# Kernel tuning notes

Hardware: AMD Instinct MI355X
Metric: run time of the kernel (lower is better)

Reference implementation:

```python
import jax, jax.numpy as jnp
import numpy as np
import math

D_MODEL, D_STATE, D_CONV = 1024, 16, 4
D_INNER = 2 * D_MODEL
DT_RANK = math.ceil(D_MODEL / 16)
B, L = 4, 2048


def setup_inputs() -> dict:
    key = jax.random.key(0)
    ks = jax.random.split(key, 10)
    s = 0.02
    x = jax.random.normal(ks[0], (B, L, D_MODEL), dtype=jnp.float32)
    ln_g = jnp.ones((D_MODEL,), jnp.float32)
    ln_b = jnp.zeros((D_MODEL,), jnp.float32)
    W_in = jax.random.normal(ks[1], (D_MODEL, 2 * D_INNER), jnp.float32) * s
    conv_w = jax.random.normal(ks[2], (D_INNER, 1, D_CONV), jnp.float32) * s
    conv_b = jnp.zeros((D_INNER,), jnp.float32)
    W_xp = jax.random.normal(ks[3], (D_INNER, DT_RANK + 2 * D_STATE), jnp.float32) * s
    W_dt = jax.random.normal(ks[4], (DT_RANK, D_INNER), jnp.float32) * (DT_RANK ** -0.5)
    # inverse-softplus of dt ~ 0.01 (between dt_min=0.001 and dt_max=0.1)
    dt_bias = jnp.full((D_INNER,), float(np.log(np.expm1(0.01))), jnp.float32)
    # S4D-real init: A = 1..d_state per channel
    A_log = jnp.log(jnp.broadcast_to(jnp.arange(1, D_STATE + 1, dtype=jnp.float32), (D_INNER, D_STATE)))
    D_skip = jnp.ones((D_INNER,), jnp.float32)
    W_out = jax.random.normal(ks[5], (D_INNER, D_MODEL), jnp.float32) * s
    return dict(x=x, ln_g=ln_g, ln_b=ln_b, W_in=W_in, conv_w=conv_w, conv_b=conv_b,
                W_xp=W_xp, W_dt=W_dt, dt_bias=dt_bias, A_log=A_log, D_skip=D_skip, W_out=W_out)


def _layernorm(x, g, b, eps=1e-5):
    m = jnp.mean(x, axis=-1, keepdims=True)
    v = jnp.mean(jnp.square(x - m), axis=-1, keepdims=True)
    return (x - m) * jax.lax.rsqrt(v + eps) * g + b


def _mamba(xn, W_in, conv_w, conv_b, W_xp, W_dt, dt_bias, A_log, D_skip, W_out):
    # xn: [B, L, d_model]
    xz = xn @ W_in                                   # [B, L, 2*d_inner]
    xi, z = jnp.split(xz, 2, axis=-1)                # each [B, L, d_inner]
    # depthwise causal conv over sequence
    xi_t = jnp.transpose(xi, (0, 2, 1))              # [B, d_inner, L]
    xc = jax.lax.conv_general_dilated(
        xi_t, conv_w, window_strides=(1,), padding=[(D_CONV - 1, 0)],
        feature_group_count=D_INNER, dimension_numbers=('NCH', 'OIH', 'NCH'))
    xc = jnp.transpose(xc, (0, 2, 1)) + conv_b       # [B, L, d_inner]
    xc = jax.nn.silu(xc)
    # input-dependent dt, B, C
    x_dbl = xc @ W_xp                                # [B, L, dt_rank + 2*d_state]
    dt_lo, Bm, Cm = jnp.split(x_dbl, [DT_RANK, DT_RANK + D_STATE], axis=-1)
    delta = jax.nn.softplus(dt_lo @ W_dt + dt_bias)  # [B, L, d_inner]
    A = -jnp.exp(A_log)                              # [d_inner, d_state]

    def step(h, inp):
        dt_t, B_t, C_t, u_t = inp                    # [B,D], [B,N], [B,N], [B,D]
        dA = jnp.exp(dt_t[..., None] * A)            # [B, D, N]
        h = h * dA + (dt_t * u_t)[..., None] * B_t[:, None, :]
        y = jnp.einsum('bdn,bn->bd', h, C_t)
        return h, y

    h0 = jnp.zeros((xn.shape[0], D_INNER, D_STATE), xn.dtype)
    inputs = (jnp.transpose(delta, (1, 0, 2)), jnp.transpose(Bm, (1, 0, 2)),
              jnp.transpose(Cm, (1, 0, 2)), jnp.transpose(xc, (1, 0, 2)))
    _, ys = jax.lax.scan(step, h0, inputs)           # ys: [L, B, d_inner]
    y = jnp.transpose(ys, (1, 0, 2)) + xc * D_skip   # [B, L, d_inner]
    y = y * jax.nn.silu(z)
    return y @ W_out                                 # [B, L, d_model]


def reference(x, ln_g, ln_b, W_in, conv_w, conv_b, W_xp, W_dt, dt_bias, A_log, D_skip, W_out):
    xn = _layernorm(x, ln_g, ln_b)
    return _mamba(xn, W_in, conv_w, conv_b, W_xp, W_dt, dt_bias, A_log, D_skip, W_out) + x
```

## Files before the change

### kernel.cpp

```cpp
#include <hip/hip_runtime.h>

#define DM 1024
#define DI 2048
#define DS 16
#define DTR 64
#define LL 2048
#define NROW 8192

typedef unsigned short u16;
typedef unsigned int u32;
typedef __bf16 bf16x8 __attribute__((ext_vector_type(8)));
typedef float f32x4 __attribute__((ext_vector_type(4)));
typedef float v2f __attribute__((ext_vector_type(2)));

__device__ __forceinline__ float bf2f(u16 u) {
  unsigned int v = ((unsigned int)u) << 16;
  return __builtin_bit_cast(float, v);
}
__device__ __forceinline__ u16 f2bf(float f) {
  unsigned int x = __builtin_bit_cast(unsigned int, f);
  x = x + 0x7fffu + ((x >> 16) & 1u);
  return (u16)(x >> 16);
}
__device__ __forceinline__ float lo_bf(u32 v) { return __builtin_bit_cast(float, v << 16); }
__device__ __forceinline__ float hi_bf(u32 v) { return __builtin_bit_cast(float, v & 0xFFFF0000u); }
__device__ __forceinline__ u32 pack_bf(float a, float b) {
  return (u32)f2bf(a) | ((u32)f2bf(b) << 16);
}
__device__ __forceinline__ bool io_f32(const u16* lng) { return lng[0] == 0; }

__device__ __forceinline__ void async16(const void* g, void* l) {
  __builtin_amdgcn_global_load_lds(
      (const __attribute__((address_space(1))) unsigned int*)g,
      (__attribute__((address_space(3))) unsigned int*)l, 16, 0, 0);
}

__device__ __forceinline__ void pow16v(float e1, v2f* E) {
  float e2 = e1 * e1;
  v2f sq = {e2, e2};
  E[0] = (v2f){e1, e2};
#pragma unroll
  for (int k = 1; k < 8; k++) E[k] = E[k - 1] * sq;
}

__device__ void transpose_dev(const void* __restrict__ in, u16* __restrict__ out,
                              int R, int C, int Cp, int bx, int by, bool f32,
                              int tid, u16 (*tile)[33]) {
  int c0 = bx * 32, r0 = by * 32;
  int tx = tid & 31, ty = tid >> 5;
#pragma unroll
  for (int i = 0; i < 4; i++) {
    int r = r0 + ty + i * 8, c = c0 + tx;
    u16 v = 0;
    if (r < R && c < C) {
      if (f32) v = f2bf(((const float*)in)[(size_t)r * C + c]);
      else     v = ((const u16*)in)[(size_t)r * C + c];
    }
    tile[ty + i * 8][tx] = v;
  }
  __syncthreads();
#pragma unroll
  for (int i = 0; i < 4; i++) {
    int oc = c0 + ty + i * 8, orr = r0 + tx;
    if (oc < Cp && orr < R) out[(size_t)oc * R + orr] = tile[tx][ty + i * 8];
  }
}

__global__ __launch_bounds__(256) void prep_k(
    const void* __restrict__ W_in, u16* __restrict__ W_inT,
    const void* __restrict__ W_dt, u16* __restrict__ W_dtT,
    const void* __restrict__ W_xp, u16* __restrict__ W_xpT,
    const void* __restrict__ W_out, u16* __restrict__ W_outT,
    const void* __restrict__ x, const u16* __restrict__ g,
    const u16* __restrict__ b, u16* __restrict__ xn) {
  __shared__ u16 tile[32][33];
  __shared__ float rs_[4], rq_[4];
  bool f32 = io_f32(g);
  int tid = threadIdx.x;
  int bid = blockIdx.x;
  if (bid < 4096) {
    transpose_dev(W_in, W_inT, 1024, 4096, 4096, bid & 127, bid >> 7, f32, tid, tile);
    return;
  } else if (bid < 4224) {
    bid -= 4096;
    transpose_dev(W_dt, W_dtT, 64, 2048, 2048, bid & 63, bid >> 6, f32, tid, tile);
    return;
  } else if (bid < 4480) {
    bid -= 4224;
    transpose_dev(W_xp, W_xpT, 2048, 96, 128, bid & 3, bid >> 2, f32, tid, tile);
    return;
  } else if (bid < 6528) {
    bid -= 4480;
    transpose_dev(W_out, W_outT, 2048, 1024, 1024, bid & 31, bid >> 5, f32, tid, tile);
    return;
  }
  int row = bid - 6528;
  float f[4];
  if (f32) {
    float4 v = ((const float4*)((const float*)x + (size_t)row * DM))[tid];
    f[0] = v.x; f[1] = v.y; f[2] = v.z; f[3] = v.w;
  } else {
    ushort4 v = ((const ushort4*)((const u16*)x + (size_t)row * DM))[tid];
    f[0] = bf2f(v.x); f[1] = bf2f(v.y); f[2] = bf2f(v.z); f[3] = bf2f(v.w);
  }
  float s = f[0] + f[1] + f[2] + f[3];
  float q = f[0] * f[0] + f[1] * f[1] + f[2] * f[2] + f[3] * f[3];
#pragma unroll
  for (int off = 32; off; off >>= 1) {
    s += __shfl_down(s, off, 64);
    q += __shfl_down(q, off, 64);
  }
  int wid = tid >> 6, lane = tid & 63;
  if (lane == 0) { rs_[wid] = s; rq_[wid] = q; }
  __syncthreads();
  float ts = rs_[0] + rs_[1] + rs_[2] + rs_[3];
  float tq = rq_[0] + rq_[1] + rq_[2] + rq_[3];
  float mean = ts * (1.f / DM);
  float var = tq * (1.f / DM) - mean * mean;
  float inv = rsqrtf(var + 1e-5f);
  int c = tid * 4;
  ushort4 o;
  u16* po = (u16*)&o;
#pragma unroll
  for (int k = 0; k < 4; k++) {
    float gk = f32 ? ((const float*)g)[c + k] : bf2f(g[c + k]);
    float bk = f32 ? ((const float*)b)[c + k] : bf2f(b[c + k]);
    po[k] = f2bf((f[k] - mean) * inv * gk + bk);
  }
  ((ushort4*)(xn + (size_t)row * DM))[tid] = o;
}

template <int EPI>
__device__ __forceinline__ void gemm_body(const u16* __restrict__ A,
                                          const u16* __restrict__ BT,
                                          void* __restrict__ C,
                                          const void* __restrict__ extra,
                                          int M, int N, int Klen, int ldk,
                                          const u16* __restrict__ lng, int mOff,
                                          u16* ldsA, u16* ldsB) {
  int tid = threadIdx.x;
  int wid = tid >> 6, lane = tid & 63;
  int l15 = lane & 15, quad = lane >> 4;
  int bm = blockIdx.x * 128;
  int bn;
  const u16* Ae = A;
  const u16* Be = BT;
  float* Cpart = nullptr;
  if (EPI == 5) {
    bn = 0;
    int ky = blockIdx.y;
    Ae += (size_t)ky * Klen;
    Be += (size_t)ky * Klen;
    Cpart = (float*)C + (size_t)ky * M * N;
  } else {
    bn = blockIdx.y * 128;
  }
  int wrow = (wid >> 1) * 64, wcol = (wid & 1) * 64;

  f32x4 zero = {0.f, 0.f, 0.f, 0.f};
  f32x4 acc[4][4];
#pragma unroll
  for (int i = 0; i < 4; i++)
#pragma unroll
    for (int j = 0; j < 4; j++) acc[i][j] = zero;

  int row0 = tid >> 2;
  int colb = (tid & 3) * 16;
  const char* Ap0 = (const char*)Ae + ((size_t)(bm + row0) * ldk) * 2 + colb;
  const char* Ap1 = (const char*)Ae + ((size_t)(bm + row0 + 64) * ldk) * 2 + colb;
  const char* Bp0 = (const char*)Be + ((size_t)(bn + row0) * ldk) * 2 + colb;
  const char* Bp1 = (const char*)Be + ((size_t)(bn + row0 + 64) * ldk) * 2 + colb;
  u16* la = ldsA + wid * 512;
  u16* lb = ldsB + wid * 512;

  for (int k0 = 0; k0 < Klen; k0 += 64) {
    size_t kb = (size_t)k0 * 2;
    async16(Ap0 + kb, la);
    async16(Ap1 + kb, la + 2048);
    async16(Ap0 + kb + 64, la + 4096);
    async16(Ap1 + kb + 64, la + 6144);
    async16(Bp0 + kb, lb);
    async16(Bp1 + kb, lb + 2048);
    async16(Bp0 + kb + 64, lb + 4096);
    async16(Bp1 + kb + 64, lb + 6144);
    __syncthreads();
#pragma unroll
    for (int s = 0; s < 2; s++) {
      bf16x8 af[4], bfr[4];
#pragma unroll
      for (int i = 0; i < 4; i++)
        af[i] = *(const bf16x8*)&ldsA[s * 4096 + (wrow + i * 16 + l15) * 32 + quad * 8];
#pragma unroll
      for (int j = 0; j < 4; j++)
        bfr[j] = *(const bf16x8*)&ldsB[s * 4096 + (wcol + j * 16 + l15) * 32 + quad * 8];
#pragma unroll
      for (int i = 0; i < 4; i++)
#pragma unroll
        for (int j = 0; j < 4; j++)
          acc[i][j] = __builtin_amdgcn_mfma_f32_16x16x32_bf16(af[i], bfr[j], acc[i][j], 0, 0, 0);
    }
    __syncthreads();
  }

  bool f32 = (EPI == 2 || EPI == 3) ? io_f32(lng) : false;
#pragma unroll
  for (int i = 0; i < 4; i++) {
#pragma unroll
    for (int j = 0; j < 4; j++) {
      int gn = bn + wcol + j * 16 + l15;
#pragma unroll
      for (int r = 0; r < 4; r++) {
        int gm = bm + wrow + i * 16 + quad * 4 + r;
        float v = acc[i][j][r];
        if (EPI == 2) {
          float bias = f32 ? ((const float*)extra)[gn] : bf2f(((const u16*)extra)[gn]);
          v += bias;
          float sp = (v > 20.f) ? v : log1pf(__expf(v));
          ((u16*)C)[(size_t)gm * N + gn] = f2bf(sp);
        } else if (EPI == 3) {
          size_t idx = (size_t)(gm + mOff) * N + gn;
          v += f32 ? ((const float*)extra)[idx] : bf2f(((const u16*)extra)[idx]);
          if (f32) ((float*)C)[idx] = v;
          else     ((u16*)C)[idx] = f2bf(v);
        } else if (EPI == 4) {
          if (gn < DI) {
            ((u16*)C)[(size_t)gm * DI + gn] = f2bf(v);
          } else {
            float sv = v / (1.f + __expf(-v));
            ((u16*)const_cast<void*>(extra))[(size_t)gm * DI + (gn - DI)] = f2bf(sv);
          }
        } else {
          Cpart[(size_t)gm * N + gn] = v;
        }
      }
    }
  }
}

#define GEMM_WRAP(name, EPI)                                                        \
  __global__ __launch_bounds__(256) void name(                                      \
      const u16* __restrict__ A, const u16* __restrict__ BT, void* __restrict__ C,  \
      const void* __restrict__ extra, int M, int N, int Klen, int ldk,              \
      const u16* __restrict__ lng, int mOff) {                                      \
    __shared__ __align__(16) u16 ldsA[128 * 64];                                    \
    __shared__ __align__(16) u16 ldsB[128 * 64];                                    \
    gemm_body<EPI>(A, BT, C, extra, M, N, Klen, ldk, lng, mOff, ldsA, ldsB);        \
  }

GEMM_WRAP(gemm_in_k, 4)
GEMM_WRAP(gemm_xp_k, 5)
GEMM_WRAP(gemm_dt_k, 2)
GEMM_WRAP(gemm_out_k, 3)

__global__ __launch_bounds__(256) void conv4_k(const u16* __restrict__ xi,
                                               const void* __restrict__ cw,
                                               const void* __restrict__ cb,
                                               u16* __restrict__ xc,
                                               const u16* __restrict__ lng) {
  bool f32 = io_f32(lng);
  int idx = blockIdx.x * 256 + threadIdx.x;
  int c = idx & (DI - 1);
  int rq = idx >> 11;
  int l4 = (rq & (LL / 4 - 1)) * 4;
  int b = rq >> 9;
  float w[4], bias;
  if (f32) {
    float4 w4 = *(const float4*)((const float*)cw + (size_t)c * 4);
    w[0] = w4.x; w[1] = w4.y; w[2] = w4.z; w[3] = w4.w;
    bias = ((const float*)cb)[c];
  } else {
    ushort4 w4 = *(const ushort4*)((const u16*)cw + (size_t)c * 4);
    w[0] = bf2f(w4.x); w[1] = bf2f(w4.y); w[2] = bf2f(w4.z); w[3] = bf2f(w4.w);
    bias = bf2f(((const u16*)cb)[c]);
  }
  size_t base = ((size_t)(b * LL + l4)) * DI + c;
  float v[7];
#pragma unroll
  for (int j = 0; j < 7; j++) {
    int lj = l4 - 3 + j;
    v[j] = (lj >= 0) ? bf2f(xi[base + (size_t)(j - 3) * DI]) : 0.f;
  }
#pragma unroll
  for (int r = 0; r < 4; r++) {
    float acc = bias + v[r] * w[0] + v[r + 1] * w[1] + v[r + 2] * w[2] + v[r + 3] * w[3];
    float sv = acc / (1.f + __expf(-acc));
    xc[base + (size_t)r * DI] = f2bf(sv);
  }
}

__global__ __launch_bounds__(256) void reduce_dtlo_k(const float* __restrict__ Cpart,
                                                     float* __restrict__ xdbl,
                                                     u16* __restrict__ dtlo, int M) {
  int i = blockIdx.x * 256 + threadIdx.x;
  size_t MN = (size_t)M * 128;
  float v = Cpart[i] + Cpart[MN + i] + Cpart[2 * MN + i] + Cpart[3 * MN + i];
  xdbl[i] = v;
  int j = i & 127, m = i >> 7;
  if (j < 64) dtlo[(size_t)m * 64 + j] = f2bf(v);
}

__device__ __forceinline__ bool fastA(const void* A_log, bool f32, int d0) {
  bool fast = true;
#pragma unroll
  for (int c = 0; c < 2; c++)
    for (int n = 0; n < 16; n++) {
      float al = f32 ? ((const float*)A_log)[(d0 + c) * DS + n]
                     : bf2f(((const u16*)A_log)[(d0 + c) * DS + n]);
      float Av = __expf(al);
      fast = fast && (__builtin_fabsf(Av - (float)(n + 1)) <= 1e-3f * (n + 1));
    }
  return fast;
}

template <int S>
__global__ __launch_bounds__(256) void scan_p1(const u16* __restrict__ delta,
                                               const u16* __restrict__ xc,
                                               const float* __restrict__ xdbl,
                                               const void* __restrict__ A_log,
                                               const u16* __restrict__ lng,
                                               float* __restrict__ Pbuf,
                                               float* __restrict__ Lbuf,
                                               int NS) {
  bool f32 = io_f32(lng);
  int tid = threadIdx.x;
  int seg = blockIdx.x, dch = blockIdx.y, bL = blockIdx.z;
  int d0 = (dch * 256 + tid) * 2;
  size_t rb = (size_t)bL * LL;
  int l0 = seg * S;
  extern __shared__ float bc[];
#pragma unroll 2
  for (int i = tid; i < S * 4; i += 256) {
    int t = i >> 2, k = (i & 3) * 4;
    *(float4*)&bc[t * 16 + k] = *(const float4*)&xdbl[(rb + l0 + t) * 128 + 64 + k];
  }
  __syncthreads();
  size_t sb = ((((size_t)bL * NS + seg) * DI) + d0) * DS;
  const u32* dpu = (const u32*)(delta + (rb + l0) * DI + d0);
  const u32* upu = (const u32*)(xc + (rb + l0) * DI + d0);
  if (fastA(A_log, f32, d0)) {
    v2f h0[8], h1[8];
#pragma unroll
    for (int k = 0; k < 8; k++) { h0[k] = (v2f){0.f, 0.f}; h1[k] = (v2f){0.f, 0.f}; }
    float sum0 = 0.f, sum1 = 0.f;
    const int T = 8;
    for (int t0 = 0; t0 < S; t0 += T) {
      u32 dv[T], uv[T];
#pragma unroll
      for (int j = 0; j < T; j++) {
        dv[j] = dpu[j * (DI / 2)];
        uv[j] = upu[j * (DI / 2)];
      }
      dpu += T * (DI / 2);
      upu += T * (DI / 2);
#pragma unroll
      for (int j = 0; j < T; j++) {
        float dt0 = lo_bf(dv[j]), dt1 = hi_bf(dv[j]);
        float u0 = lo_bf(uv[j]), u1 = hi_bf(uv[j]);
        sum0 += dt0; sum1 += dt1;
        const v2f* B2 = (const v2f*)&bc[(t0 + j) * 16];
        v2f E[8];
        pow16v(__expf(-dt0), E);
        float com0 = dt0 * u0;
        v2f cv0 = {com0, com0};
#pragma unroll
        for (int k = 0; k < 8; k++) h0[k] = h0[k] * E[k] + B2[k] * cv0;
        pow16v(__expf(-dt1), E);
        float com1 = dt1 * u1;
        v2f cv1 = {com1, com1};
#pragma unroll
        for (int k = 0; k < 8; k++) h1[k] = h1[k] * E[k] + B2[k] * cv1;
      }
    }
    v2f P[8];
    pow16v(__expf(-sum0), P);
#pragma unroll
    for (int k = 0; k < 8; k++) { *(v2f*)&Pbuf[sb + 2 * k] = P[k]; *(v2f*)&Lbuf[sb + 2 * k] = h0[k]; }
    pow16v(__expf(-sum1), P);
#pragma unroll
    for (int k = 0; k < 8; k++) { *(v2f*)&Pbuf[sb + 16 + 2 * k] = P[k]; *(v2f*)&Lbuf[sb + 16 + 2 * k] = h1[k]; }
  } else {
    for (int c = 0; c < 2; c++) {
      int d = d0 + c;
      float A2[16], h[16], P[16];
#pragma unroll
      for (int n = 0; n < 16; n++) {
        float al = f32 ? ((const float*)A_log)[d * DS + n] : bf2f(((const u16*)A_log)[d * DS + n]);
        A2[n] = -__expf(al);
        h[n] = 0.f; P[n] = 1.f;
      }
      const u16* dp = delta + (rb + l0) * DI + d;
      const u16* up = xc + (rb + l0) * DI + d;
      for (int t = 0; t < S; t++) {
        float dt = bf2f(dp[(size_t)t * DI]);
        float u = bf2f(up[(size_t)t * DI]);
        float com = dt * u;
        const float* Bf = &bc[t * 16];
#pragma unroll
        for (int n = 0; n < 16; n++) {
          float dA = __expf(dt * A2[n]);
          h[n] = fmaf(h[n], dA, com * Bf[n]);
          P[n] *= dA;
        }
      }
#pragma unroll
      for (int n = 0; n < 16; n++) { Pbuf[sb + 16 * c + n] = P[n]; Lbuf[sb + 16 * c + n] = h[n]; }
    }
  }
}

__global__ __launch_bounds__(256) void scan_p2(float* __restrict__ Pbuf,
                                               float* __restrict__ Lbuf, int NS) {
  int idx = blockIdx.x * 256 + threadIdx.x;
  int bL = idx >> 15;
  int dn = idx & 32767;
  float H = 0.f;
  for (int s = 0; s < NS; s++) {
    size_t o = ((size_t)(bL * NS + s) << 15) + dn;
    float P = Pbuf[o], Lv = Lbuf[o];
    Lbuf[o] = H;
    H = fmaf(P, H, Lv);
  }
}

template <int S>
__global__ __launch_bounds__(256) void scan_p3(u16* __restrict__ dy,
                                               const u16* __restrict__ xc,
                                               const float* __restrict__ xdbl,
                                               const u16* __restrict__ z,
                                               const void* __restrict__ A_log,
                                               const void* __restrict__ D_skip,
                                               const u16* __restrict__ lng,
                                               const float* __restrict__ Lbuf,
                                               int NS) {
  bool f32 = io_f32(lng);
  int tid = threadIdx.x;
  int seg = blockIdx.x, dch = blockIdx.y, bL = blockIdx.z;
  int d0 = (dch * 256 + tid) * 2;
  size_t rb = (size_t)bL * LL;
  int l0 = seg * S;
  extern __shared__ float bc[];
#pragma unroll 2
  for (int i = tid; i < S * 8; i += 256) {
    int t = i >> 3, k = (i & 7) * 4;
    *(float4*)&bc[t * 32 + k] = *(const float4*)&xdbl[(rb + l0 + t) * 128 + 64 + k];
  }
  __syncthreads();
  size_t sb = ((((size_t)bL * NS + seg) * DI) + d0) * DS;
  float Dv0 = f32 ? ((const float*)D_skip)[d0] : bf2f(((const u16*)D_skip)[d0]);
  float Dv1 = f32 ? ((const float*)D_skip)[d0 + 1] : bf2f(((const u16*)D_skip)[d0 + 1]);
  u32* dpu = (u32*)(dy + (rb + l0) * DI + d0);
  const u32* upu = (const u32*)(xc + (rb + l0) * DI + d0);
  const u32* zpu = (const u32*)(z + (rb + l0) * DI + d0);
  if (fastA(A_log, f32, d0)) {
    v2f h0[8], h1[8];
#pragma unroll
    for (int k = 0; k < 8; k++) {
      h0[k] = *(const v2f*)&Lbuf[sb + 2 * k];
      h1[k] = *(const v2f*)&Lbuf[sb + 16 + 2 * k];
    }
    const int T = 8;
    for (int t0 = 0; t0 < S; t0 += T) {
      u32 dv[T], uv[T], zv[T];
#pragma unroll
      for (int j = 0; j < T; j++) {
        dv[j] = dpu[j * (DI / 2)];
        uv[j] = upu[j * (DI / 2)];
        zv[j] = zpu[j * (DI / 2)];
      }
      upu += T * (DI / 2);
      zpu += T * (DI / 2);
#pragma unroll
      for (int j = 0; j < T; j++) {
        float dt0 = lo_bf(dv[j]), dt1 = hi_bf(dv[j]);
        float u0 = lo_bf(uv[j]), u1 = hi_bf(uv[j]);
        float zg0 = lo_bf(zv[j]), zg1 = hi_bf(zv[j]);
        const v2f* B2 = (const v2f*)&bc[(t0 + j) * 32];
        const v2f* C2 = (const v2f*)&bc[(t0 + j) * 32 + 16];
        v2f E[8];
        pow16v(__expf(-dt0), E);
        float com0 = dt0 * u0;
        v2f cv = {com0, com0};
        v2f a0 = {0.f, 0.f}, a1 = {0.f, 0.f};
#pragma unroll
        for (int k = 0; k < 8; k += 2) {
          h0[k] = h0[k] * E[k] + B2[k] * cv;
          h0[k + 1] = h0[k + 1] * E[k + 1] + B2[k + 1] * cv;
          a0 += h0[k] * C2[k];
          a1 += h0[k + 1] * C2[k + 1];
        }
        float cs0 = (a0.x + a0.y) + (a1.x + a1.y);
        pow16v(__expf(-dt1), E);
        float com1 = dt1 * u1;
        cv = (v2f){com1, com1};
        a0 = (v2f){0.f, 0.f}; a1 = (v2f){0.f, 0.f};
#pragma unroll
        for (int k = 0; k < 8; k += 2) {
          h1[k] = h1[k] * E[k] + B2[k] * cv;
          h1[k + 1] = h1[k + 1] * E[k + 1] + B2[k + 1] * cv;
          a0 += h1[k] * C2[k];
          a1 += h1[k + 1] * C2[k + 1];
        }
        float cs1 = (a0.x + a0.y) + (a1.x + a1.y);
        float y0 = (cs0 + u0 * Dv0) * zg0;
        float y1 = (cs1 + u1 * Dv1) * zg1;
        dpu[j * (DI / 2)] = pack_bf(y0, y1);
      }
      dpu += T * (DI / 2);
    }
  } else {
    for (int c = 0; c < 2; c++) {
      int d = d0 + c;
      float A2[16], h[16];
#pragma unroll
      for (int n = 0; n < 16; n++) {
        float al = f32 ? ((const float*)A_log)[d * DS + n] : bf2f(((const u16*)A_log)[d * DS + n]);
        A2[n] = -__expf(al);
        h[n] = Lbuf[sb + 16 * c + n];
      }
      float Dv = (c == 0) ? Dv0 : Dv1;
      u16* dp = dy + (rb + l0) * DI + d;
      const u16* up = xc + (rb + l0) * DI + d;
      const u16* zp = z + (rb + l0) * DI + d;
      for (int t = 0; t < S; t++) {
        float dt = bf2f(dp[(size_t)t * DI]);
        float u = bf2f(up[(size_t)t * DI]);
        float zg = bf2f(zp[(size_t)t * DI]);
        float com = dt * u;
        const float* Bf = &bc[t * 32];
        const float* Cf = &bc[t * 32 + 16];
        float cs = 0.f;
#pragma unroll
        for (int n = 0; n < 16; n++) {
          float dA = __expf(dt * A2[n]);
          h[n] = fmaf(h[n], dA, com * Bf[n]);
          cs = fmaf(h[n], Cf[n], cs);
        }
        dp[(size_t)t * DI] = f2bf((cs + u * Dv) * zg);
      }
    }
  }
}

static void launch_scan(int NS, int nb, u16* xi, u16* xc, float* xdbl, u16* z,
                        const u16* A_log, const u16* D_sk, const u16* ln_g,
                        float* Pbuf, float* Lbuf, hipStream_t stream) {
  int S = LL / NS;
  dim3 g1(NS, 4, nb);
  if (S == 32) {
    scan_p1<32><<<g1, 256, 32 * 64, stream>>>(xi, xc, xdbl, A_log, ln_g, Pbuf, Lbuf, NS);
  } else if (S == 64) {
    scan_p1<64><<<g1, 256, 64 * 64, stream>>>(xi, xc, xdbl, A_log, ln_g, Pbuf, Lbuf, NS);
  } else {
    scan_p1<128><<<g1, 256, 128 * 64, stream>>>(xi, xc, xdbl, A_log, ln_g, Pbuf, Lbuf, NS);
  }
  scan_p2<<<nb * 128, 256, 0, stream>>>(Pbuf, Lbuf, NS);
  if (S == 32) {
    scan_p3<32><<<g1, 256, 32 * 128, stream>>>(xi, xc, xdbl, z, A_log, D_sk, ln_g, Lbuf, NS);
  } else if (S == 64) {
    scan_p3<64><<<g1, 256, 64 * 128, stream>>>(xi, xc, xdbl, z, A_log, D_sk, ln_g, Lbuf, NS);
  } else {
    scan_p3<128><<<g1, 256, 128 * 128, stream>>>(xi, xc, xdbl, z, A_log, D_sk, ln_g, Lbuf, NS);
  }
}

extern "C" void kernel_launch(void* const* d_in, const int* in_sizes, int n_in,
                              void* d_out, int out_size, void* d_ws, size_t ws_size,
                              hipStream_t stream) {
  const u16* x = (const u16*)d_in[0];
  const u16* ln_g = (const u16*)d_in[1];
  const u16* ln_b = (const u16*)d_in[2];
  const u16* W_in = (const u16*)d_in[3];
  const u16* cw = (const u16*)d_in[4];
  const u16* cb = (const u16*)d_in[5];
  const u16* W_xp = (const u16*)d_in[6];
  const u16* W_dt = (const u16*)d_in[7];
  const u16* dt_b = (const u16*)d_in[8];
  const u16* A_log = (const u16*)d_in[9];
  const u16* D_sk = (const u16*)d_in[10];
  const u16* W_out = (const u16*)d_in[11];

  char* ws = (char*)d_ws;
  const size_t MB = 1024 * 1024;

  if (ws_size >= 124 * MB) {
    int NS = (ws_size >= 180 * MB) ? 64 : (ws_size >= 144 * MB) ? 32 : 16;
    u16* xc = (u16*)(ws + 0);
    u16* xn = xc;
    u16* W_inT = (u16*)(ws + 16 * MB);
    u16* xi = (u16*)(ws + 32 * MB);
    u16* z = (u16*)(ws + 64 * MB);
    float* xdbl = (float*)(ws + 96 * MB);
    u16* dtlo = (u16*)(ws + 100 * MB);
    u16* W_xpT = (u16*)(ws + 101 * MB);
    u16* W_dtT = (u16*)(ws + 102 * MB);
    u16* W_outT = (u16*)(ws + 103 * MB);
    size_t stateSz = (size_t)NS * 4 * DI * DS * 4;
    float* Cpart = (float*)(ws + 107 * MB);
    float* Pbuf = (float*)(ws + 107 * MB);
    float* Lbuf = (float*)(ws + 107 * MB + stateSz);

    prep_k<<<6528 + NROW, 256, 0, stream>>>(W_in, W_inT, W_dt, W_dtT, W_xp, W_xpT,
                                            W_out, W_outT, x, ln_g, ln_b, xn);
    gemm_in_k<<<dim3(64, 32), 256, 0, stream>>>(xn, W_inT, xi, z, NROW, 2 * DI, DM, DM, ln_g, 0);
    conv4_k<<<(NROW / 4 * DI) / 256, 256, 0, stream>>>(xi, cw, cb, xc, ln_g);
    gemm_xp_k<<<dim3(64, 4), 256, 0, stream>>>(xc, W_xpT, Cpart, nullptr, NROW, 128, 512, DI, ln_g, 0);
    reduce_dtlo_k<<<(NROW * 128) / 256, 256, 0, stream>>>(Cpart, xdbl, dtlo, NROW);
    gemm_dt_k<<<dim3(64, 16), 256, 0, stream>>>(dtlo, W_dtT, xi, dt_b, NROW, DI, DTR, DTR, ln_g, 0);
    launch_scan(NS, 4, xi, xc, xdbl, z, A_log, D_sk, ln_g, Pbuf, Lbuf, stream);
    gemm_out_k<<<dim3(64, 8), 256, 0, stream>>>(xi, W_outT, d_out, x, NROW, DM, DI, DI, ln_g, 0);
  } else {
    int NS = 32;
    u16* W_inT = (u16*)(ws + 0);
    u16* W_xpT = (u16*)(ws + 8 * MB);
    u16* W_dtT = (u16*)(ws + 9 * MB);
    u16* W_outT = (u16*)(ws + 10 * MB);
    u16* xn = (u16*)(ws + 14 * MB);
    u16* xi = (u16*)(ws + 30 * MB);
    u16* z = (u16*)(ws + 38 * MB);
    u16* xc = (u16*)(ws + 46 * MB);
    float* xdbl = (float*)(ws + 54 * MB);
    u16* dtlo = (u16*)(ws + 55 * MB);
    float* Cpart = (float*)(ws + 56 * MB);
    float* Pbuf = (float*)(ws + 56 * MB);
    float* Lbuf = (float*)(ws + 61 * MB);

    prep_k<<<6528 + NROW, 256, 0, stream>>>(W_in, W_inT, W_dt, W_dtT, W_xp, W_xpT,
                                            W_out, W_outT, x, ln_g, ln_b, xn);
    for (int b = 0; b < 4; b++) {
      const u16* xnb = xn + (size_t)b * LL * DM;
      gemm_in_k<<<dim3(16, 32), 256, 0, stream>>>(xnb, W_inT, xi, z, LL, 2 * DI, DM, DM, ln_g, 0);
      conv4_k<<<(LL / 4 * DI) / 256, 256, 0, stream>>>(xi, cw, cb, xc, ln_g);
      gemm_xp_k<<<dim3(16, 4), 256, 0, stream>>>(xc, W_xpT, Cpart, nullptr, LL, 128, 512, DI, ln_g, 0);
      reduce_dtlo_k<<<(LL * 128) / 256, 256, 0, stream>>>(Cpart, xdbl, dtlo, LL);
      gemm_dt_k<<<dim3(16, 16), 256, 0, stream>>>(dtlo, W_dtT, xi, dt_b, LL, DI, DTR, DTR, ln_g, 0);
      launch_scan(NS, 1, xi, xc, xdbl, z, A_log, D_sk, ln_g, Pbuf, Lbuf, stream);
      gemm_out_k<<<dim3(16, 8), 256, 0, stream>>>(xi, W_outT, d_out, x, LL, DM, DI, DI, ln_g, b * LL);
    }
  }
}
```

Before: 529.1 us.

## Add dedicated 256x256-tile in-projection GEMM with pipelined async LDS loads

Replaces the generic 128x128 in-projection GEMM with a specialized 512-thread kernel that computes 256x256 output tiles. Global-to-LDS loads are asynchronous and double-buffered and interleaved with quarter-tile MFMA phases, with s_setprio raising priority during math. The larger tile raises arithmetic intensity and reduces redundant global loads. The cost is heavier register and LDS use (128 KB LDS per block) and fewer blocks to fill the GPU.

```diff
diff --git a/kernel.cpp b/kernel.cpp
--- a/kernel.cpp
+++ b/kernel.cpp
@@ -222,13 +222,6 @@
           v += f32 ? ((const float*)extra)[idx] : bf2f(((const u16*)extra)[idx]);
           if (f32) ((float*)C)[idx] = v;
           else     ((u16*)C)[idx] = f2bf(v);
-        } else if (EPI == 4) {
-          if (gn < DI) {
-            ((u16*)C)[(size_t)gm * DI + gn] = f2bf(v);
-          } else {
-            float sv = v / (1.f + __expf(-v));
-            ((u16*)const_cast<void*>(extra))[(size_t)gm * DI + (gn - DI)] = f2bf(sv);
-          }
         } else {
           Cpart[(size_t)gm * N + gn] = v;
         }
@@ -247,10 +240,177 @@
     gemm_body<EPI>(A, BT, C, extra, M, N, Klen, ldk, lng, mOff, ldsA, ldsB);        \
   }
 
-GEMM_WRAP(gemm_in_k, 4)
 GEMM_WRAP(gemm_xp_k, 5)
 GEMM_WRAP(gemm_dt_k, 2)
 GEMM_WRAP(gemm_out_k, 3)
+
+__global__ __launch_bounds__(512, 2) void gemm_in256_k(
+    const u16* __restrict__ A, const u16* __restrict__ BT,
+    u16* __restrict__ C, u16* __restrict__ Z, int ldk, int Klen) {
+  __shared__ __align__(16) u16 lds[65536];
+  const int tid = threadIdx.x;
+  const int wid = tid >> 6, lane = tid & 63;
+  const int l15 = lane & 15, quad = lane >> 4;
+  const int bm = blockIdx.x * 256, bn = blockIdx.y * 256;
+  const int wrow = (wid >> 2) * 128;
+  const int wcol = (wid & 3) * 64;
+
+  const int srow = tid >> 3;
+  const int sg = ((tid & 7) ^ (srow & 7)) * 8;
+  const u16* Ag[4];
+  const u16* Bg[4];
+#pragma unroll
+  for (int s = 0; s < 4; s++) {
+    Ag[s] = A + (size_t)(bm + s * 64 + srow) * ldk + sg;
+    Bg[s] = BT + (size_t)(bn + s * 64 + srow) * ldk + sg;
+  }
+  const int sdst = wid * 512;
+
+  int rA[2], rB[2];
+#pragma unroll
+  for (int ks = 0; ks < 2; ks++) {
+    int gsw = ((ks * 4 + quad) ^ (l15 & 7)) * 8;
+    rA[ks] = (wrow + l15) * 64 + gsw;
+    rB[ks] = 16384 + (wcol + l15) * 64 + gsw;
+  }
+
+  f32x4 acc[8][4];
+  f32x4 zero = {0.f, 0.f, 0.f, 0.f};
+#pragma unroll
+  for (int i = 0; i < 8; i++)
+#pragma unroll
+    for (int j = 0; j < 4; j++) acc[i][j] = zero;
+
+  const int NT = Klen >> 6;
+  async16(Ag[0], &lds[sdst]);
+  async16(Ag[1], &lds[4096 + sdst]);
+  async16(Bg[0], &lds[16384 + sdst]);
+  async16(Bg[1], &lds[16384 + 4096 + sdst]);
+  async16(Bg[2], &lds[16384 + 8192 + sdst]);
+  async16(Bg[3], &lds[16384 + 12288 + sdst]);
+  async16(Ag[2], &lds[8192 + sdst]);
+  async16(Ag[3], &lds[12288 + sdst]);
+  if (NT > 1) {
+    async16(Ag[0] + 64, &lds[32768 + sdst]);
+    async16(Ag[1] + 64, &lds[32768 + 4096 + sdst]);
+  }
+
+  bf16x8 a[4][2], b0[2][2], b1[2][2];
+  for (int t = 0; t < NT; ++t) {
+    const int bb = (t & 1) << 15;
+    const int nb = bb ^ 32768;
+    const int k1 = (t + 1) << 6;
+    const int k2 = (t + 2) << 6;
+    const bool st1 = (t + 1 < NT), st2 = (t + 2 < NT);
+    if (st1) asm volatile("s_waitcnt vmcnt(2)" ::: "memory");
+    else     asm volatile("s_waitcnt vmcnt(0)" ::: "memory");
+    __builtin_amdgcn_s_barrier();
+
+#pragma unroll
+    for (int mf = 0; mf < 4; mf++) {
+      a[mf][0] = *(const bf16x8*)&lds[bb + rA[0] + mf * 1024];
+      a[mf][1] = *(const bf16x8*)&lds[bb + rA[1] + mf * 1024];
+    }
+#pragma unroll
+    for (int nf = 0; nf < 2; nf++) {
+      b0[nf][0] = *(const bf16x8*)&lds[bb + rB[0] + nf * 1024];
+      b0[nf][1] = *(const bf16x8*)&lds[bb + rB[1] + nf * 1024];
+    }
+    if (st1) {
+      async16(Bg[0] + k1, &lds[nb + 16384 + sdst]);
+      async16(Bg[1] + k1, &lds[nb + 16384 + 4096 + sdst]);
+    }
+    __builtin_amdgcn_s_barrier();
+    asm volatile("s_waitcnt lgkmcnt(0)" ::: "memory");
+    __builtin_amdgcn_s_setprio(1);
+#pragma unroll
+    for (int ks = 0; ks < 2; ks++)
+#pragma unroll
+      for (int mf = 0; mf < 4; mf++)
+#pragma unroll
+        for (int nf = 0; nf < 2; nf++)
+          acc[mf][nf] = __builtin_amdgcn_mfma_f32_16x16x32_bf16(a[mf][ks], b0[nf][ks], acc[mf][nf], 0, 0, 0);
+    __builtin_amdgcn_s_setprio(0);
+    __builtin_amdgcn_s_barrier();
+
+#pragma unroll
+    for (int nf = 0; nf < 2; nf++) {
+      b1[nf][0] = *(const bf16x8*)&lds[bb + rB[0] + (2 + nf) * 1024];
+      b1[nf][1] = *(const bf16x8*)&lds[bb + rB[1] + (2 + nf) * 1024];
+    }
+    if (st1) {
+      async16(Bg[2] + k1, &lds[nb + 16384 + 8192 + sdst]);
+      async16(Bg[3] + k1, &lds[nb + 16384 + 12288 + sdst]);
+    }
+    __builtin_amdgcn_s_barrier();
+    asm volatile("s_waitcnt lgkmcnt(0)" ::: "memory");
+    __builtin_amdgcn_s_setprio(1);
+#pragma unroll
+    for (int ks = 0; ks < 2; ks++)
+#pragma unroll
+      for (int mf = 0; mf < 4; mf++)
+#pragma unroll
+        for (int nf = 0; nf < 2; nf++)
+          acc[mf][2 + nf] = __builtin_amdgcn_mfma_f32_16x16x32_bf16(a[mf][ks], b1[nf][ks], acc[mf][2 + nf], 0, 0, 0);
+    __builtin_amdgcn_s_setprio(0);
+    __builtin_amdgcn_s_barrier();
+
+#pragma unroll
+    for (int mf = 0; mf < 4; mf++) {
+      a[mf][0] = *(const bf16x8*)&lds[bb + rA[0] + 4096 + mf * 1024];
+      a[mf][1] = *(const bf16x8*)&lds[bb + rA[1] + 4096 + mf * 1024];
+    }
+    if (st1) {
+      async16(Ag[2] + k1, &lds[nb + 8192 + sdst]);
+      async16(Ag[3] + k1, &lds[nb + 12288 + sdst]);
+    }
+    __builtin_amdgcn_s_barrier();
+    asm volatile("s_waitcnt lgkmcnt(0)" ::: "memory");
+    __builtin_amdgcn_s_setprio(1);
+#pragma unroll
+    for (int ks = 0; ks < 2; ks++)
+#pragma unroll
+      for (int mf = 0; mf < 4; mf++)
+#pragma unroll
+        for (int nf = 0; nf < 2; nf++)
+          acc[4 + mf][2 + nf] = __builtin_amdgcn_mfma_f32_16x16x32_bf16(a[mf][ks], b1[nf][ks], acc[4 + mf][2 + nf], 0, 0, 0);
+    __builtin_amdgcn_s_setprio(0);
+    __builtin_amdgcn_s_barrier();
+
+    if (st2) {
+      async16(Ag[0] + k2, &lds[bb + sdst]);
+      async16(Ag[1] + k2, &lds[bb + 4096 + sdst]);
+    }
+    __builtin_amdgcn_s_setprio(1);
+#pragma unroll
+    for (int ks = 0; ks < 2; ks++)
+#pragma unroll
+      for (int mf = 0; mf < 4; mf++)
+#pragma unroll
+        for (int nf = 0; nf < 2; nf++)
+          acc[4 + mf][nf] = __builtin_amdgcn_mfma_f32_16x16x32_bf16(a[mf][ks], b0[nf][ks], acc[4 + mf][nf], 0, 0, 0);
+    __builtin_amdgcn_s_setprio(0);
+  }
+
+#pragma unroll
+  for (int i = 0; i < 8; i++) {
+#pragma unroll
+    for (int j = 0; j < 4; j++) {
+      int gn = bn + wcol + j * 16 + l15;
+#pragma unroll
+      for (int r = 0; r < 4; r++) {
+        int gm = bm + wrow + i * 16 + quad * 4 + r;
+        float v = acc[i][j][r];
+        if (gn < DI) {
+          C[(size_t)gm * DI + gn] = f2bf(v);
+        } else {
+          float sv = v / (1.f + __expf(-v));
+          Z[(size_t)gm * DI + (gn - DI)] = f2bf(sv);
+        }
+      }
+    }
+  }
+}
 
 __global__ __launch_bounds__(256) void conv4_k(const u16* __restrict__ xi,
                                                const void* __restrict__ cw,
@@ -601,7 +761,7 @@
 
     prep_k<<<6528 + NROW, 256, 0, stream>>>(W_in, W_inT, W_dt, W_dtT, W_xp, W_xpT,
                                             W_out, W_outT, x, ln_g, ln_b, xn);
-    gemm_in_k<<<dim3(64, 32), 256, 0, stream>>>(xn, W_inT, xi, z, NROW, 2 * DI, DM, DM, ln_g, 0);
+    gemm_in256_k<<<dim3(NROW / 256, (2 * DI) / 256), 512, 0, stream>>>(xn, W_inT, xi, z, DM, DM);
     conv4_k<<<(NROW / 4 * DI) / 256, 256, 0, stream>>>(xi, cw, cb, xc, ln_g);
     gemm_xp_k<<<dim3(64, 4), 256, 0, stream>>>(xc, W_xpT, Cpart, nullptr, NROW, 128, 512, DI, ln_g, 0);
     reduce_dtlo_k<<<(NROW * 128) / 256, 256, 0, stream>>>(Cpart, xdbl, dtlo, NROW);
@@ -628,7 +788,7 @@
                                             W_out, W_outT, x, ln_g, ln_b, xn);
     for (int b = 0; b < 4; b++) {
       const u16* xnb = xn + (size_t)b * LL * DM;
-      gemm_in_k<<<dim3(16, 32), 256, 0, stream>>>(xnb, W_inT, xi, z, LL, 2 * DI, DM, DM, ln_g, 0);
+      gemm_in256_k<<<dim3(LL / 256, (2 * DI) / 256), 512, 0, stream>>>(xnb, W_inT, xi, z, DM, DM);
       conv4_k<<<(LL / 4 * DI) / 256, 256, 0, stream>>>(xi, cw, cb, xc, ln_g);
       gemm_xp_k<<<dim3(16, 4), 256, 0, stream>>>(xc, W_xpT, Cpart, nullptr, LL, 128, 512, DI, ln_g, 0);
       reduce_dtlo_k<<<(LL * 128) / 256, 256, 0, stream>>>(Cpart, xdbl, dtlo, LL);
```

Result: no change. 523.6 us (-1.0%).
